# Kernel optimization log

Measured on AMD Instinct MI355X. Metric: run time of the kernel, lower is better.

## Reference

```python
import jax, jax.numpy as jnp
import numpy as np

N_NODES = 100000
N_EDGES = 1600000
IN_F = 128
HID_F = 128
OUT_F = 128

def _glorot(key, shape):
    lim = np.sqrt(6.0 / (shape[0] + shape[1]))
    return jax.random.uniform(key, shape, jnp.float32, -lim, lim)

def setup_inputs() -> dict:
    key = jax.random.key(0)
    ks = jax.random.split(key, 9)
    x = jax.random.normal(ks[0], (N_NODES, IN_F), jnp.float32)
    src = jax.random.randint(ks[1], (N_EDGES,), 0, N_NODES, jnp.int32)
    dst = jax.random.randint(ks[2], (N_EDGES,), 0, N_NODES, jnp.int32)
    return {
        'x': x, 'src': src, 'dst': dst,
        'W_self1': _glorot(ks[3], (IN_F, HID_F)),
        'W_neigh1': _glorot(ks[4], (IN_F, HID_F)),
        'b1': jnp.zeros((HID_F,), jnp.float32),
        'W_self2': _glorot(ks[5], (HID_F, OUT_F)),
        'W_neigh2': _glorot(ks[6], (HID_F, OUT_F)),
        'b2': jnp.zeros((OUT_F,), jnp.float32),
    }

def _sage_mean(h, src, dst, W_self, W_neigh, b, n_nodes):
    # mean-aggregate src features onto dst (DGL SAGEConv 'mean')
    msg_sum = jax.ops.segment_sum(h[src], dst, num_segments=n_nodes)  # [N, d]
    deg = jax.ops.segment_sum(jnp.ones_like(dst, jnp.float32), dst, num_segments=n_nodes)
    h_neigh = msg_sum / jnp.maximum(deg, 1.0)[:, None]
    return h @ W_self + h_neigh @ W_neigh + b

def reference(x, src, dst, W_self1, W_neigh1, b1, W_self2, W_neigh2, b2):
    n = x.shape[0]
    h = _sage_mean(x, src, dst, W_self1, W_neigh1, b1, n)
    h = _sage_mean(h, src, dst, W_self2, W_neigh2, b2, n)
    # edge-wise dot product score between endpoint features (u_dot_v)
    s = jnp.sum(h[src] * h[dst], axis=-1)  # [E]
    smin, smax = jnp.min(s), jnp.max(s)
    return (s - smin) / (smax - smin)
```

## Files before the change

### kernel.cpp

```cpp
#include <hip/hip_runtime.h>
#include <hip/hip_bf16.h>

#define F 128

typedef unsigned int uint;
typedef unsigned short ushort;
typedef __attribute__((ext_vector_type(8))) short short8;
typedef __attribute__((ext_vector_type(4))) float f32x4;

__device__ inline ushort f2bf(float f) {
    uint u = __float_as_uint(f);
    u += 0x7FFF + ((u >> 16) & 1);
    return (ushort)(u >> 16);
}
__device__ inline float2 bf2f(uint u) {
    return make_float2(__uint_as_float(u << 16), __uint_as_float(u & 0xFFFF0000u));
}
__device__ inline void acc8(float* a, uint4 v) {
    float2 f;
    f = bf2f(v.x); a[0] += f.x; a[1] += f.y;
    f = bf2f(v.y); a[2] += f.x; a[3] += f.y;
    f = bf2f(v.z); a[4] += f.x; a[5] += f.y;
    f = bf2f(v.w); a[6] += f.x; a[7] += f.y;
}
__device__ inline void unp8(float* a, uint4 v) {
    float2 f;
    f = bf2f(v.x); a[0] = f.x; a[1] = f.y;
    f = bf2f(v.y); a[2] = f.x; a[3] = f.y;
    f = bf2f(v.z); a[4] = f.x; a[5] = f.y;
    f = bf2f(v.w); a[6] = f.x; a[7] = f.y;
}
__device__ inline float dot8(const float* d, uint4 v) {
    float2 f; float s = 0.f;
    f = bf2f(v.x); s += f.x * d[0] + f.y * d[1];
    f = bf2f(v.y); s += f.x * d[2] + f.y * d[3];
    f = bf2f(v.z); s += f.x * d[4] + f.y * d[5];
    f = bf2f(v.w); s += f.x * d[6] + f.y * d[7];
    return s;
}

__global__ __launch_bounds__(256) void rank_kernel(const int* __restrict__ dst,
                                                   int* __restrict__ cnt,
                                                   ushort* __restrict__ rel, int E) {
    int e = blockIdx.x * 256 + threadIdx.x;
    if (e < E) rel[e] = (ushort)atomicAdd(&cnt[dst[e]], 1);
}

__global__ __launch_bounds__(256) void scan_block(const int* __restrict__ cnt,
                                                  int* __restrict__ off,
                                                  int* __restrict__ bsum, int N) {
    __shared__ int t[256];
    int i = blockIdx.x * 256 + threadIdx.x;
    int v = (i < N) ? cnt[i] : 0;
    t[threadIdx.x] = v;
    __syncthreads();
    for (int o = 1; o < 256; o <<= 1) {
        int x = (threadIdx.x >= o) ? t[threadIdx.x - o] : 0;
        __syncthreads();
        t[threadIdx.x] += x;
        __syncthreads();
    }
    if (i < N) off[i] = t[threadIdx.x] - v;
    if (threadIdx.x == 255) bsum[blockIdx.x] = t[255];
}

__global__ __launch_bounds__(512) void scan_sums(int* __restrict__ bsum, int nb) {
    __shared__ int t[512];
    int v = (threadIdx.x < nb) ? bsum[threadIdx.x] : 0;
    t[threadIdx.x] = v;
    __syncthreads();
    for (int o = 1; o < 512; o <<= 1) {
        int x = (threadIdx.x >= o) ? t[threadIdx.x - o] : 0;
        __syncthreads();
        t[threadIdx.x] += x;
        __syncthreads();
    }
    if (threadIdx.x < nb) bsum[threadIdx.x] = t[threadIdx.x] - v;
}

__global__ __launch_bounds__(256) void scan_add_rdeg(int* __restrict__ off,
                                                     const int* __restrict__ bsum,
                                                     const int* __restrict__ cnt,
                                                     float* __restrict__ rdeg, int N) {
    int i = blockIdx.x * 256 + threadIdx.x;
    if (i >= N) return;
    off[i] += bsum[blockIdx.x];
    rdeg[i] = 1.0f / fmaxf((float)cnt[i], 1.0f);
}

__global__ __launch_bounds__(256) void fill_kernel(const int* __restrict__ src,
                                                   const int* __restrict__ dst,
                                                   const int* __restrict__ off,
                                                   const ushort* __restrict__ rel,
                                                   int* __restrict__ srcS, int E) {
    int e = blockIdx.x * 256 + threadIdx.x;
    if (e >= E) return;
    srcS[off[dst[e]] + (int)rel[e]] = src[e];
}

__global__ __launch_bounds__(256) void prep_kernel(const float* __restrict__ x,
                                                   const float* __restrict__ W0,
                                                   const float* __restrict__ W1,
                                                   const float* __restrict__ W2,
                                                   const float* __restrict__ W3,
                                                   uint* __restrict__ xb,
                                                   ushort* __restrict__ Wt, int NF4, int N) {
    int i = blockIdx.x * 256 + threadIdx.x;
    if (i < NF4) {
        float4 v = ((const float4*)x)[i];
        uint ua = (uint)f2bf(v.x) | ((uint)f2bf(v.y) << 16);
        uint ub = (uint)f2bf(v.z) | ((uint)f2bf(v.w) << 16);
        int r = i >> 5;
        int g = i & 31;
        int c = g >> 2;
        int o = (g & 3) * 2;
        uint* dstp = xb + (size_t)c * (size_t)N * 8 + (size_t)r * 8 + o;
        *(uint2*)dstp = make_uint2(ua, ub);
    } else {
        int idx = i - NF4;
        if (idx >= 4 * 16384) return;
        int mat = idx >> 14;
        int pos = idx & 16383;
        int k = pos >> 7, n = pos & 127;
        const float* W = (mat == 0) ? W0 : (mat == 1) ? W1 : (mat == 2) ? W2 : W3;
        Wt[mat * 16384 + n * 128 + k] = f2bf(W[k * 128 + n]);
    }
}

__global__ __launch_bounds__(256) void agg_gather_cm(const uint* __restrict__ hb,
                                                     const int* __restrict__ off,
                                                     const int* __restrict__ srcS,
                                                     const float* __restrict__ rdeg,
                                                     uint* __restrict__ msgb,
                                                     int N, int E) {
    int chunk = blockIdx.x & 7;
    int ngrp = blockIdx.x >> 3;
    int lane = threadIdx.x & 63;
    int t = lane & 7;
    int g = lane >> 3;
    int slot = t >> 1;
    int half = t & 1;
    int node = ngrp * 32 + (threadIdx.x >> 6) * 8 + g;
    if (node >= N) return;
    const uint* hc = hb + (size_t)chunk * (size_t)N * 8;
    int p = off[node];
    int pe = (node == N - 1) ? E : off[node + 1];
    float acc[8];
#pragma unroll
    for (int j = 0; j < 8; j++) acc[j] = 0.f;
    if (p < pe) {
        int deg = pe - p;
        int last = pe - 1;
        for (; p < pe; p += 8) {
            int ia = min(p + slot, last);
            int ib = min(p + 4 + slot, last);
            int sa = srcS[ia], sb = srcS[ib];
            uint4 va = *(const uint4*)(hc + (size_t)sa * 8 + half * 4);
            uint4 vb = *(const uint4*)(hc + (size_t)sb * 8 + half * 4);
            acc8(acc, va);
            acc8(acc, vb);
        }
        int d = (8 - (deg & 7)) & 7;
        if (d && slot == 0) {
            uint4 vl = *(const uint4*)(hc + (size_t)srcS[last] * 8 + half * 4);
            float tmp[8];
            unp8(tmp, vl);
            float fd = (float)d;
#pragma unroll
            for (int j = 0; j < 8; j++) acc[j] -= fd * tmp[j];
        }
    }
#pragma unroll
    for (int j = 0; j < 8; j++) {
        acc[j] += __shfl_xor(acc[j], 2);
        acc[j] += __shfl_xor(acc[j], 4);
    }
    if (slot == 0) {
        float rd = rdeg[node];
        uint4 w;
        w.x = (uint)f2bf(acc[0] * rd) | ((uint)f2bf(acc[1] * rd) << 16);
        w.y = (uint)f2bf(acc[2] * rd) | ((uint)f2bf(acc[3] * rd) << 16);
        w.z = (uint)f2bf(acc[4] * rd) | ((uint)f2bf(acc[5] * rd) << 16);
        w.w = (uint)f2bf(acc[6] * rd) | ((uint)f2bf(acc[7] * rd) << 16);
        *(uint4*)(msgb + (size_t)chunk * (size_t)N * 8 + (size_t)node * 8 + half * 4) = w;
    }
}

__global__ __launch_bounds__(256) void sage_mfma(const uint* __restrict__ hb,
                                                 const uint* __restrict__ mb,
                                                 const uint* __restrict__ Wt,
                                                 const float* __restrict__ bias,
                                                 ushort* __restrict__ outb, int N) {
    int wave = threadIdx.x >> 6, lane = threadIdx.x & 63;
    int m = lane & 15, q = lane >> 4;
    int r0 = blockIdx.x * 64 + wave * 16;
    int arow = r0 + m;
    if (arow >= N) arow = N - 1;

    f32x4 acc[8];
#pragma unroll
    for (int t = 0; t < 8; t++) acc[t] = (f32x4){0.f, 0.f, 0.f, 0.f};

    size_t N8 = (size_t)N * 8;
#pragma unroll
    for (int sel = 0; sel < 2; sel++) {
        const uint* arowp = (sel ? mb : hb) + (size_t)arow * 8 + (q & 1) * 4;
        const uint* wsel = Wt + sel * 8192;
#pragma unroll
        for (int kk = 0; kk < 4; kk++) {
            short8 a = *(const short8*)(arowp + (size_t)(kk * 2 + (q >> 1)) * N8);
            int ko = kk * 16 + q * 4;
#pragma unroll
            for (int t = 0; t < 8; t++) {
                short8 b = *(const short8*)(wsel + (size_t)(16 * t + m) * 64 + ko);
                acc[t] = __builtin_amdgcn_mfma_f32_16x16x32_bf16(a, b, acc[t], 0, 0, 0);
            }
        }
    }

#pragma unroll
    for (int t = 0; t < 8; t++) {
        float bs = bias[16 * t + m];
#pragma unroll
        for (int r = 0; r < 4; r++) {
            int orow = r0 + q * 4 + r;
            if (orow < N)
                outb[(size_t)t * (size_t)N * 16 + (size_t)orow * 16 + m] = f2bf(acc[t][r] + bs);
        }
    }
}

__global__ __launch_bounds__(256) void edge_part(const uint* __restrict__ hb,
                                                 const int* __restrict__ off,
                                                 const int* __restrict__ srcS,
                                                 float* __restrict__ pbuf,
                                                 int N, int E) {
    int chunk = blockIdx.x & 7;
    int ngrp = blockIdx.x >> 3;
    int lane = threadIdx.x & 63;
    int t = lane & 7;
    int g = lane >> 3;
    int slot = t >> 1;
    int half = t & 1;
    int node = ngrp * 32 + (threadIdx.x >> 6) * 8 + g;
    if (node >= N) return;
    const uint* hc = hb + (size_t)chunk * (size_t)N * 8;
    float* pb = pbuf + (size_t)chunk * (size_t)E;
    int p = off[node];
    int pe = (node == N - 1) ? E : off[node + 1];
    if (p >= pe) return;

    float dF[8];
    unp8(dF, *(const uint4*)(hc + (size_t)node * 8 + half * 4));

    int last = pe - 1;
    for (; p < pe; p += 8) {
        int ia = min(p + slot, last);
        int ib = min(p + 4 + slot, last);
        int sa = srcS[ia], sb = srcS[ib];
        uint4 va = *(const uint4*)(hc + (size_t)sa * 8 + half * 4);
        uint4 vb = *(const uint4*)(hc + (size_t)sb * 8 + half * 4);
        float pa = dot8(dF, va);
        float pc = dot8(dF, vb);
        pa += __shfl_xor(pa, 1);
        pc += __shfl_xor(pc, 1);
        if (half == 0) {
            if (p + slot <= last) pb[p + slot] = pa;
            if (p + 4 + slot <= last) pb[p + 4 + slot] = pc;
        }
    }
}

__global__ __launch_bounds__(256) void fold_minmax(const float* __restrict__ pbuf,
                                                   float* __restrict__ sc,
                                                   float2* __restrict__ pmm, int E) {
    int i = blockIdx.x * 256 + threadIdx.x;
    float lmin = INFINITY, lmax = -INFINITY;
    if (i < E) {
        float v = 0.f;
#pragma unroll
        for (int c = 0; c < 8; c++) v += pbuf[(size_t)c * (size_t)E + i];
        sc[i] = v;
        lmin = lmax = v;
    }
#pragma unroll
    for (int o = 1; o <= 32; o <<= 1) {
        lmin = fminf(lmin, __shfl_xor(lmin, o));
        lmax = fmaxf(lmax, __shfl_xor(lmax, o));
    }
    __shared__ float smin[4], smax[4];
    int lane = threadIdx.x & 63, wv = threadIdx.x >> 6;
    if (lane == 0) { smin[wv] = lmin; smax[wv] = lmax; }
    __syncthreads();
    if (threadIdx.x == 0) {
        float mA = fminf(fminf(smin[0], smin[1]), fminf(smin[2], smin[3]));
        float MA = fmaxf(fmaxf(smax[0], smax[1]), fmaxf(smax[2], smax[3]));
        pmm[blockIdx.x] = make_float2(mA, MA);
    }
}

__global__ __launch_bounds__(1024) void minmax_final(const float2* __restrict__ pmm,
                                                     float* __restrict__ mmf, int nb) {
    float vmin = INFINITY, vmax = -INFINITY;
    for (int i = threadIdx.x; i < nb; i += 1024) {
        float2 v = pmm[i];
        vmin = fminf(vmin, v.x);
        vmax = fmaxf(vmax, v.y);
    }
#pragma unroll
    for (int o = 1; o <= 32; o <<= 1) {
        vmin = fminf(vmin, __shfl_xor(vmin, o));
        vmax = fmaxf(vmax, __shfl_xor(vmax, o));
    }
    __shared__ float smin[16], smax[16];
    int lane = threadIdx.x & 63, wv = threadIdx.x >> 6;
    if (lane == 0) { smin[wv] = vmin; smax[wv] = vmax; }
    __syncthreads();
    if (threadIdx.x == 0) {
        float m = smin[0], M = smax[0];
        for (int w = 1; w < 16; w++) { m = fminf(m, smin[w]); M = fmaxf(M, smax[w]); }
        mmf[0] = m;
        mmf[1] = M;
    }
}

__global__ __launch_bounds__(256) void norm_kernel(const float* __restrict__ sc,
                                                   const int* __restrict__ dst,
                                                   const ushort* __restrict__ rel,
                                                   const int* __restrict__ off,
                                                   float* __restrict__ out,
                                                   const float* __restrict__ mmf, int E) {
    float mn = mmf[0];
    float mx = mmf[1];
    float inv = 1.0f / (mx - mn);
    int i = blockIdx.x * 256 + threadIdx.x;
    if (i < E) {
        int p = off[dst[i]] + (int)rel[i];
        out[i] = (sc[p] - mn) * inv;
    }
}

extern "C" void kernel_launch(void* const* d_in, const int* in_sizes, int n_in,
                              void* d_out, int out_size, void* d_ws, size_t ws_size,
                              hipStream_t stream) {
    const float* x   = (const float*)d_in[0];
    const int*   src = (const int*)d_in[1];
    const int*   dst = (const int*)d_in[2];
    const float* Ws1 = (const float*)d_in[3];
    const float* Wn1 = (const float*)d_in[4];
    const float* b1  = (const float*)d_in[5];
    const float* Ws2 = (const float*)d_in[6];
    const float* Wn2 = (const float*)d_in[7];
    const float* b2  = (const float*)d_in[8];

    int N = in_sizes[0] / F;
    int E = in_sizes[1];
    float* out = (float*)d_out;

    int nbN = (N + 255) / 256;
    int nbE = (E + 255) / 256;
    int NF4 = N * F / 4;

    int* off  = (int*)d_ws;
    int* cnt  = off + N;
    int* srcS = cnt + N;
    ushort* rel = (ushort*)(srcS + E);
    float* sc = (float*)((int*)rel + E / 2);
    int* bsum = (int*)(sc + E);
    float* rdeg = (float*)(bsum + 1024);
    float* mmf = (float*)(rdeg + N);
    float2* pmm = (float2*)(mmf + 4);
    uint* Wtb = (uint*)(pmm + 25600);
    size_t elemOff = 3 * (size_t)N + 2 * (size_t)E + (size_t)E / 2 + 1024 + 4 + 51200 + 32768;
    elemOff = (elemOff + 3) & ~(size_t)3;
    uint* xb   = (uint*)d_ws + elemOff;
    uint* msgb = xb + (size_t)N * 64;
    uint* h1b  = msgb + (size_t)N * 64;
    uint* h2b  = h1b + (size_t)N * 64;
    float* pbuf = (float*)xb;

    hipMemsetAsync(cnt, 0, (size_t)N * sizeof(int), stream);

    rank_kernel<<<nbE, 256, 0, stream>>>(dst, cnt, rel, E);
    scan_block<<<nbN, 256, 0, stream>>>(cnt, off, bsum, N);
    scan_sums<<<1, 512, 0, stream>>>(bsum, nbN);
    scan_add_rdeg<<<nbN, 256, 0, stream>>>(off, bsum, cnt, rdeg, N);
    fill_kernel<<<nbE, 256, 0, stream>>>(src, dst, off, rel, srcS, E);

    prep_kernel<<<(NF4 + 4 * 16384 + 255) / 256, 256, 0, stream>>>(
        x, Ws1, Wn1, Ws2, Wn2, xb, (ushort*)Wtb, NF4, N);

    int nbAgg = 8 * ((N + 31) / 32);

    agg_gather_cm<<<nbAgg, 256, 0, stream>>>(xb, off, srcS, rdeg, msgb, N, E);
    sage_mfma<<<(N + 63) / 64, 256, 0, stream>>>(xb, msgb, Wtb, b1, (ushort*)h1b, N);

    agg_gather_cm<<<nbAgg, 256, 0, stream>>>(h1b, off, srcS, rdeg, msgb, N, E);
    sage_mfma<<<(N + 63) / 64, 256, 0, stream>>>(h1b, msgb, Wtb + 16384, b2, (ushort*)h2b, N);

    edge_part<<<nbAgg, 256, 0, stream>>>(h2b, off, srcS, pbuf, N, E);
    fold_minmax<<<nbE, 256, 0, stream>>>(pbuf, sc, pmm, E);
    minmax_final<<<1, 1024, 0, stream>>>(pmm, mmf, nbE);
    norm_kernel<<<nbE, 256, 0, stream>>>(sc, dst, rel, off, out, mmf, E);
}
```

Before: 634.8 us.

## Fuse edge dot scoring with min/max and pre-swizzle weights for MFMA

Replaces the CSR-ordered per-chunk edge partial kernel and the fold pass with a single edge-order kernel. Each thread gathers the src and dst rows across all eight channel chunks, staggered per XCD, and emits the score plus per-block min/max. This removes the 8xE partial buffer and the permuted index lookups in the normalize step, which becomes a vectorized float4 pass. Separately, the weights are pre-arranged into MFMA fragment order so each lane loads B contiguously. The cost is two random row gathers per edge in original edge order with no reuse of the dst row, and norm4 assumes E is divisible by 4.

```diff
diff --git a/kernel.cpp b/kernel.cpp
--- a/kernel.cpp
+++ b/kernel.cpp
@@ -2,6 +2,8 @@
 #include <hip/hip_bf16.h>
 
 #define F 128
+#define EPT 4
+#define EPB (256 * EPT)
 
 typedef unsigned int uint;
 typedef unsigned short ushort;
@@ -30,12 +32,12 @@
     f = bf2f(v.z); a[4] = f.x; a[5] = f.y;
     f = bf2f(v.w); a[6] = f.x; a[7] = f.y;
 }
-__device__ inline float dot8(const float* d, uint4 v) {
-    float2 f; float s = 0.f;
-    f = bf2f(v.x); s += f.x * d[0] + f.y * d[1];
-    f = bf2f(v.y); s += f.x * d[2] + f.y * d[3];
-    f = bf2f(v.z); s += f.x * d[4] + f.y * d[5];
-    f = bf2f(v.w); s += f.x * d[6] + f.y * d[7];
+__device__ inline float dpair(uint4 a, uint4 b) {
+    float2 fa, fb; float s = 0.f;
+    fa = bf2f(a.x); fb = bf2f(b.x); s += fa.x * fb.x + fa.y * fb.y;
+    fa = bf2f(a.y); fb = bf2f(b.y); s += fa.x * fb.x + fa.y * fb.y;
+    fa = bf2f(a.z); fb = bf2f(b.z); s += fa.x * fb.x + fa.y * fb.y;
+    fa = bf2f(a.w); fb = bf2f(b.w); s += fa.x * fb.x + fa.y * fb.y;
     return s;
 }
 
@@ -119,11 +121,15 @@
     } else {
         int idx = i - NF4;
         if (idx >= 4 * 16384) return;
-        int mat = idx >> 14;
-        int pos = idx & 16383;
-        int k = pos >> 7, n = pos & 127;
+        int j    = idx & 7;
+        int lane = (idx >> 3) & 63;
+        int t    = (idx >> 9) & 7;
+        int kk   = (idx >> 12) & 3;
+        int mat  = idx >> 14;
+        int n = 16 * t + (lane & 15);
+        int k = 32 * kk + 8 * (lane >> 4) + j;
         const float* W = (mat == 0) ? W0 : (mat == 1) ? W1 : (mat == 2) ? W2 : W3;
-        Wt[mat * 16384 + n * 128 + k] = f2bf(W[k * 128 + n]);
+        Wt[idx] = f2bf(W[k * 128 + n]);
     }
 }
 
@@ -209,10 +215,9 @@
 #pragma unroll
         for (int kk = 0; kk < 4; kk++) {
             short8 a = *(const short8*)(arowp + (size_t)(kk * 2 + (q >> 1)) * N8);
-            int ko = kk * 16 + q * 4;
 #pragma unroll
             for (int t = 0; t < 8; t++) {
-                short8 b = *(const short8*)(wsel + (size_t)(16 * t + m) * 64 + ko);
+                short8 b = *(const short8*)(wsel + (size_t)((kk * 8 + t) * 64 + lane) * 4);
                 acc[t] = __builtin_amdgcn_mfma_f32_16x16x32_bf16(a, b, acc[t], 0, 0, 0);
             }
         }
@@ -230,58 +235,47 @@
     }
 }
 
-__global__ __launch_bounds__(256) void edge_part(const uint* __restrict__ hb,
-                                                 const int* __restrict__ off,
-                                                 const int* __restrict__ srcS,
-                                                 float* __restrict__ pbuf,
-                                                 int N, int E) {
-    int chunk = blockIdx.x & 7;
-    int ngrp = blockIdx.x >> 3;
-    int lane = threadIdx.x & 63;
-    int t = lane & 7;
-    int g = lane >> 3;
-    int slot = t >> 1;
-    int half = t & 1;
-    int node = ngrp * 32 + (threadIdx.x >> 6) * 8 + g;
-    if (node >= N) return;
-    const uint* hc = hb + (size_t)chunk * (size_t)N * 8;
-    float* pb = pbuf + (size_t)chunk * (size_t)E;
-    int p = off[node];
-    int pe = (node == N - 1) ? E : off[node + 1];
-    if (p >= pe) return;
-
-    float dF[8];
-    unp8(dF, *(const uint4*)(hc + (size_t)node * 8 + half * 4));
-
-    int last = pe - 1;
-    for (; p < pe; p += 8) {
-        int ia = min(p + slot, last);
-        int ib = min(p + 4 + slot, last);
-        int sa = srcS[ia], sb = srcS[ib];
-        uint4 va = *(const uint4*)(hc + (size_t)sa * 8 + half * 4);
-        uint4 vb = *(const uint4*)(hc + (size_t)sb * 8 + half * 4);
-        float pa = dot8(dF, va);
-        float pc = dot8(dF, vb);
-        pa += __shfl_xor(pa, 1);
-        pc += __shfl_xor(pc, 1);
-        if (half == 0) {
-            if (p + slot <= last) pb[p + slot] = pa;
-            if (p + 4 + slot <= last) pb[p + 4 + slot] = pc;
-        }
-    }
-}
-
-__global__ __launch_bounds__(256) void fold_minmax(const float* __restrict__ pbuf,
-                                                   float* __restrict__ sc,
-                                                   float2* __restrict__ pmm, int E) {
-    int i = blockIdx.x * 256 + threadIdx.x;
+__global__ __launch_bounds__(256) void edge_dot(const uint* __restrict__ hb,
+                                                const int* __restrict__ src,
+                                                const int* __restrict__ dst,
+                                                float* __restrict__ sc,
+                                                float2* __restrict__ pmm, int N, int E) {
+    int xcd = blockIdx.x & 7;
+    int ebase = blockIdx.x * EPB + threadIdx.x;
+    int si[EPT], di[EPT];
+    float acc[EPT];
+#pragma unroll
+    for (int j = 0; j < EPT; j++) {
+        int e = ebase + j * 256;
+        int ec = (e < E) ? e : E - 1;
+        si[j] = src[ec];
+        di[j] = dst[ec];
+        acc[j] = 0.f;
+    }
+    size_t N8 = (size_t)N * 8;
+    for (int cc = 0; cc < 8; cc++) {
+        int c = (cc + xcd) & 7;
+        const uint* hc = hb + (size_t)c * N8;
+#pragma unroll
+        for (int j = 0; j < EPT; j++) {
+            const uint* sp = hc + (size_t)si[j] * 8;
+            const uint* dp = hc + (size_t)di[j] * 8;
+            uint4 a0 = *(const uint4*)sp;
+            uint4 a1 = *(const uint4*)(sp + 4);
+            uint4 b0 = *(const uint4*)dp;
+            uint4 b1 = *(const uint4*)(dp + 4);
+            acc[j] += dpair(a0, b0) + dpair(a1, b1);
+        }
+    }
     float lmin = INFINITY, lmax = -INFINITY;
-    if (i < E) {
-        float v = 0.f;
-#pragma unroll
-        for (int c = 0; c < 8; c++) v += pbuf[(size_t)c * (size_t)E + i];
-        sc[i] = v;
-        lmin = lmax = v;
+#pragma unroll
+    for (int j = 0; j < EPT; j++) {
+        int e = ebase + j * 256;
+        if (e < E) {
+            sc[e] = acc[j];
+            lmin = fminf(lmin, acc[j]);
+            lmax = fmaxf(lmax, acc[j]);
+        }
     }
 #pragma unroll
     for (int o = 1; o <= 32; o <<= 1) {
@@ -324,20 +318,19 @@
     }
 }
 
-__global__ __launch_bounds__(256) void norm_kernel(const float* __restrict__ sc,
-                                                   const int* __restrict__ dst,
-                                                   const ushort* __restrict__ rel,
-                                                   const int* __restrict__ off,
-                                                   float* __restrict__ out,
-                                                   const float* __restrict__ mmf, int E) {
+__global__ __launch_bounds__(256) void norm4_kernel(const float* __restrict__ sc,
+                                                    float* __restrict__ out,
+                                                    const float* __restrict__ mmf, int E4) {
+    int i = blockIdx.x * 256 + threadIdx.x;
+    if (i >= E4) return;
     float mn = mmf[0];
-    float mx = mmf[1];
-    float inv = 1.0f / (mx - mn);
-    int i = blockIdx.x * 256 + threadIdx.x;
-    if (i < E) {
-        int p = off[dst[i]] + (int)rel[i];
-        out[i] = (sc[p] - mn) * inv;
-    }
+    float inv = 1.0f / (mmf[1] - mn);
+    float4 v = ((const float4*)sc)[i];
+    v.x = (v.x - mn) * inv;
+    v.y = (v.y - mn) * inv;
+    v.z = (v.z - mn) * inv;
+    v.w = (v.w - mn) * inv;
+    ((float4*)out)[i] = v;
 }
 
 extern "C" void kernel_launch(void* const* d_in, const int* in_sizes, int n_in,
@@ -377,7 +370,6 @@
     uint* msgb = xb + (size_t)N * 64;
     uint* h1b  = msgb + (size_t)N * 64;
     uint* h2b  = h1b + (size_t)N * 64;
-    float* pbuf = (float*)xb;
 
     hipMemsetAsync(cnt, 0, (size_t)N * sizeof(int), stream);
 
@@ -398,8 +390,8 @@
     agg_gather_cm<<<nbAgg, 256, 0, stream>>>(h1b, off, srcS, rdeg, msgb, N, E);
     sage_mfma<<<(N + 63) / 64, 256, 0, stream>>>(h1b, msgb, Wtb + 16384, b2, (ushort*)h2b, N);
 
-    edge_part<<<nbAgg, 256, 0, stream>>>(h2b, off, srcS, pbuf, N, E);
-    fold_minmax<<<nbE, 256, 0, stream>>>(pbuf, sc, pmm, E);
-    minmax_final<<<1, 1024, 0, stream>>>(pmm, mmf, nbE);
-    norm_kernel<<<nbE, 256, 0, stream>>>(sc, dst, rel, off, out, mmf, E);
-}
+    int nbDot = (E + EPB - 1) / EPB;
+    edge_dot<<<nbDot, 256, 0, stream>>>(h2b, src, dst, sc, pmm, N, E);
+    minmax_final<<<1, 1024, 0, stream>>>(pmm, mmf, nbDot);
+    norm4_kernel<<<(E / 4 + 255) / 256, 256, 0, stream>>>(sc, out, mmf, E / 4);
+}
```

Result: slower. 779.7 us (+22.8%).
